# Performance work log

Hardware: AMD Instinct MI355X
Metric: run time of the kernel (lower is better)

## Reference

```python
import jax, jax.numpy as jnp
import numpy as np

HEADS = 8
DIM_HEAD = 64  # scale uses this, even though per-head dim is 128 (inner_dim = dim_head*heads*2)
SCALE = DIM_HEAD ** (-0.5)
QUERY_DIM = 1024
COND_DIM = 1024
INNER_DIM = DIM_HEAD * HEADS * 2  # 1024


def setup_inputs() -> dict:
    key = jax.random.key(0)
    ks = jax.random.split(key, 7)
    B, Nq, Nk = 4, 2048, 2048
    x = jax.random.normal(ks[0], (B, Nq, QUERY_DIM), dtype=jnp.float32)
    cond = jax.random.normal(ks[1], (B, Nk, COND_DIM), dtype=jnp.float32)
    s = 0.02
    Wq = jax.random.normal(ks[2], (QUERY_DIM, INNER_DIM), dtype=jnp.float32) * s
    Wk = jax.random.normal(ks[3], (COND_DIM, INNER_DIM), dtype=jnp.float32) * s
    Wv = jax.random.normal(ks[4], (COND_DIM, INNER_DIM), dtype=jnp.float32) * s
    Wo = jax.random.normal(ks[5], (INNER_DIM, QUERY_DIM), dtype=jnp.float32) * s
    bo = jax.random.normal(ks[6], (QUERY_DIM,), dtype=jnp.float32) * s
    return {"x": x, "cond": cond, "Wq": Wq, "Wk": Wk, "Wv": Wv, "Wo": Wo, "bo": bo}


def reference(x, cond, Wq, Wk, Wv, Wo, bo):
    B, Nq, _ = x.shape
    Nk = cond.shape[1]
    h = HEADS
    d = INNER_DIM // h  # 128 per-head dim
    q = (x @ Wq).reshape(B, Nq, h, d).transpose(0, 2, 1, 3)   # b h i d
    k = (cond @ Wk).reshape(B, Nk, h, d).transpose(0, 2, 1, 3)  # b h j d
    v = (cond @ Wv).reshape(B, Nk, h, d).transpose(0, 2, 1, 3)  # b h j d
    sim = jnp.einsum('bhid,bhjd->bhij', q, k) * SCALE
    attn = jax.nn.softmax(sim, axis=-1)
    out = jnp.einsum('bhij,bhjd->bhid', attn, v)
    out = out.transpose(0, 2, 1, 3).reshape(B, Nq, INNER_DIM)
    return out @ Wo + bo
```

## Files before the change

### kernel.cpp

```cpp
#include <hip/hip_runtime.h>
#include <cstdint>
#include <cstddef>


typedef __attribute__((ext_vector_type(8))) __bf16 bf16x8;
typedef __attribute__((ext_vector_type(4))) float  f32x4;

__device__ __forceinline__ unsigned short f2bf(float f) {
  union { float f; unsigned u; } v; v.f = f;
  unsigned r = v.u + 0x7FFFu + ((v.u >> 16) & 1u);
  return (unsigned short)(r >> 16);
}

__device__ __forceinline__ void async_copy16(const void* g, void* l) {
  __builtin_amdgcn_global_load_lds(
      (const __attribute__((address_space(1))) void*)g,
      (__attribute__((address_space(3))) void*)l, 16, 0, 0);
}

__device__ __forceinline__ void tile_ready_barrier() {
  __builtin_amdgcn_sched_barrier(0);
  asm volatile("s_waitcnt vmcnt(0)" ::: "memory");
  __builtin_amdgcn_s_barrier();
  __builtin_amdgcn_sched_barrier(0);
}

__global__ void convert2_f32_bf16(const float* __restrict__ a,
                                  unsigned short* __restrict__ ao,
                                  const float* __restrict__ b,
                                  unsigned short* __restrict__ bo, int n4) {
  const float* in = blockIdx.z ? b : a;
  unsigned short* out = blockIdx.z ? bo : ao;
  int idx = blockIdx.x * blockDim.x + threadIdx.x;
  int stride = gridDim.x * blockDim.x;
  for (int i = idx; i < n4; i += stride) {
    float4 v = ((const float4*)in)[i];
    ushort4 o;
    o.x = f2bf(v.x); o.y = f2bf(v.y); o.z = f2bf(v.z); o.w = f2bf(v.w);
    ((ushort4*)out)[i] = o;
  }
}

__global__ void tconv4(const float* __restrict__ W0, const float* __restrict__ W1,
                       const float* __restrict__ W2, const float* __restrict__ W3,
                       unsigned short* __restrict__ T0, unsigned short* __restrict__ T1,
                       unsigned short* __restrict__ T2, unsigned short* __restrict__ T3) {
  const int Kd = 1024, Nd = 1024;
  int z = blockIdx.z;
  const float* W = (z == 0) ? W0 : (z == 1) ? W1 : (z == 2) ? W2 : W3;
  unsigned short* Wt = (z == 0) ? T0 : (z == 1) ? T1 : (z == 2) ? T2 : T3;
  __shared__ float t[32][33];
  int tx = threadIdx.x, ty = threadIdx.y;
  int n0 = blockIdx.x * 32, k0 = blockIdx.y * 32;
#pragma unroll
  for (int i = 0; i < 4; ++i)
    t[ty + i * 8][tx] = W[(size_t)(k0 + ty + i * 8) * Nd + n0 + tx];
  __syncthreads();
#pragma unroll
  for (int i = 0; i < 4; ++i)
    Wt[(size_t)(n0 + ty + i * 8) * Kd + k0 + tx] = f2bf(t[tx][ty + i * 8]);
}

template <int MODE>
__global__ __launch_bounds__(256, 3) void gemm_bt(
    const unsigned short* __restrict__ A, const unsigned short* __restrict__ Bt,
    void* __restrict__ Cp, const float* __restrict__ bias, int M, int N, int Kd,
    float oscale) {
  __shared__ __align__(16) unsigned short As[2][128 * 32];
  __shared__ __align__(16) unsigned short Bs[2][128 * 32];
  int tid = threadIdx.x, lane = tid & 63, wid = tid >> 6;
  int wm = wid >> 1, wn = wid & 1;
  int nwg = gridDim.x * gridDim.y;
  int wg = blockIdx.y * gridDim.x + blockIdx.x;
  int cpx = nwg >> 3;
  int sw = (wg & 7) * cpx + (wg >> 3);
  int bx = sw % gridDim.x, by = sw / gridDim.x;
  int m0 = by * 128, n0 = bx * 128;
  int l15 = lane & 15, g = lane >> 4;
  const unsigned short* Ag = A + (size_t)m0 * Kd;
  const unsigned short* Bg = Bt + (size_t)n0 * Kd;
  f32x4 acc[4][4] = {};

  auto stage = [&](int buf, int k0) {
#pragma unroll
    for (int it = 0; it < 2; ++it) {
      int c = it * 256 + tid;
      int row = c >> 2, kg = c & 3;
      async_copy16(Ag + (size_t)row * Kd + k0 + kg * 8, &As[buf][c * 8]);
      async_copy16(Bg + (size_t)row * Kd + k0 + kg * 8, &Bs[buf][c * 8]);
    }
  };

  const int NT = Kd >> 5;
  stage(0, 0);

  for (int t = 0; t < NT; ++t) {
    tile_ready_barrier();
    if (t + 1 < NT) stage((t + 1) & 1, (t + 1) * 32);
    int cur = t & 1;
    bf16x8 af[4], bfr[4];
#pragma unroll
    for (int i = 0; i < 4; ++i) {
      af[i]  = *(const bf16x8*)(&As[cur][(wm * 64 + i * 16 + l15) * 32 + g * 8]);
      bfr[i] = *(const bf16x8*)(&Bs[cur][(wn * 64 + i * 16 + l15) * 32 + g * 8]);
    }
    __builtin_amdgcn_s_setprio(1);
#pragma unroll
    for (int i = 0; i < 4; ++i)
#pragma unroll
      for (int j = 0; j < 4; ++j)
        acc[i][j] = __builtin_amdgcn_mfma_f32_16x16x32_bf16(af[i], bfr[j], acc[i][j], 0, 0, 0);
    __builtin_amdgcn_s_setprio(0);
  }

#pragma unroll
  for (int i = 0; i < 4; ++i) {
#pragma unroll
    for (int j = 0; j < 4; ++j) {
#pragma unroll
      for (int r = 0; r < 4; ++r) {
        int row = m0 + wm * 64 + i * 16 + g * 4 + r;
        int col = n0 + wn * 64 + j * 16 + l15;
        float v = acc[i][j][r];
        if (MODE == 0) {
          ((unsigned short*)Cp)[(size_t)row * N + col] = f2bf(v * oscale);
        } else if (MODE == 1) {
          ((float*)Cp)[(size_t)row * N + col] = v + bias[col];
        } else {
          size_t off = ((size_t)((col >> 11) * 8 + (row >> 7)) << 18) +
                       (size_t)(row & 127) * 2048 + (size_t)(col & 2047);
          ((unsigned short*)Cp)[off] = f2bf(v);
        }
      }
    }
  }
}

#define KVB 64
#define NKV 2048

__global__ __launch_bounds__(512, 4) void attn_kernel(
    const unsigned short* __restrict__ Q, const unsigned short* __restrict__ K,
    const unsigned short* __restrict__ Vt, unsigned short* __restrict__ O) {
  __shared__ __align__(16) unsigned short Ks[2][KVB * 128];
  __shared__ __align__(16) unsigned short Vs[2][128 * KVB];
  __shared__ __align__(16) unsigned short Ps[8 * 16 * 64];

  int tid = threadIdx.x, lane = tid & 63, w = tid >> 6;
  int l15 = lane & 15, g = lane >> 4;
  int wgl = blockIdx.y * gridDim.x + blockIdx.x;
  int sw = (wgl & 7) * 64 + (wgl >> 3);
  int bh = sw >> 4, b = bh >> 3, h = bh & 7;
  int q0 = (sw & 15) * 128;

  const unsigned short* Qg = Q + ((size_t)(b * 2048 + q0 + w * 16)) * 1024 + h * 128;
  const unsigned short* Kg = K + ((size_t)(b * 2048)) * 1024 + h * 128;
  const unsigned short* Vg = Vt + (size_t)bh * (128 * 2048);

  bf16x8 qf[4];
#pragma unroll
  for (int kf = 0; kf < 4; ++kf)
    qf[kf] = *(const bf16x8*)(Qg + (size_t)l15 * 1024 + kf * 32 + g * 8);

  f32x4 of[8] = {};
  float mrun[4], lrun[4];
#pragma unroll
  for (int r = 0; r < 4; ++r) { mrun[r] = -1e30f; lrun[r] = 0.f; }

  auto stage = [&](int buf, int j0) {
#pragma unroll
    for (int it = 0; it < 2; ++it) {
      int c = it * 512 + tid;
      int row = c >> 4, kc = c & 15;
      async_copy16(Kg + (size_t)(j0 + row) * 1024 + ((kc ^ (row & 7)) * 8),
                   &Ks[buf][c * 8]);
    }
#pragma unroll
    for (int it = 0; it < 2; ++it) {
      int c = it * 512 + tid;
      int row = c >> 3, jc = c & 7;
      async_copy16(Vg + (size_t)row * 2048 + j0 + ((jc ^ (row & 7)) * 8),
                   &Vs[buf][c * 8]);
    }
  };

  const int NT = NKV / KVB;
  stage(0, 0);

  for (int t = 0; t < NT; ++t) {
    tile_ready_barrier();
    if (t + 1 < NT) stage((t + 1) & 1, (t + 1) * KVB);
    int cur = t & 1;

    f32x4 s[4] = {};
    __builtin_amdgcn_s_setprio(1);
#pragma unroll
    for (int jf = 0; jf < 4; ++jf) {
      int j = jf * 16 + l15;
#pragma unroll
      for (int kf = 0; kf < 4; ++kf) {
        bf16x8 kfr = *(const bf16x8*)(&Ks[cur][j * 128 + (((kf * 4 + g) ^ (j & 7)) * 8)]);
        s[jf] = __builtin_amdgcn_mfma_f32_16x16x32_bf16(qf[kf], kfr, s[jf], 0, 0, 0);
      }
    }
    __builtin_amdgcn_s_setprio(0);

#pragma unroll
    for (int r = 0; r < 4; ++r) {
      float mxl = fmaxf(fmaxf(s[0][r], s[1][r]), fmaxf(s[2][r], s[3][r]));
      if (!__all(mxl <= mrun[r] + 11.5f)) {
        float mx = mxl;
#pragma unroll
        for (int msk = 1; msk < 16; msk <<= 1) mx = fmaxf(mx, __shfl_xor(mx, msk, 64));
        float mnew = fmaxf(mrun[r], mx);
        float resc = __builtin_amdgcn_exp2f(mrun[r] - mnew);
        lrun[r] *= resc;
#pragma unroll
        for (int df = 0; df < 8; ++df) of[df][r] *= resc;
        mrun[r] = mnew;
      }
      float ps = 0.f;
      float pj[4];
#pragma unroll
      for (int jf = 0; jf < 4; ++jf) {
        pj[jf] = __builtin_amdgcn_exp2f(s[jf][r] - mrun[r]);
        ps += pj[jf];
      }
      lrun[r] += ps;
      int prow = g * 4 + r;
#pragma unroll
      for (int jf = 0; jf < 4; ++jf) {
        int idx = (w * 16 + prow) * 64 +
                  (((jf * 2 + (l15 >> 3)) ^ (prow & 7)) << 3) + (l15 & 7);
        Ps[idx] = f2bf(pj[jf]);
      }
    }

    bf16x8 pa[2];
#pragma unroll
    for (int kf2 = 0; kf2 < 2; ++kf2)
      pa[kf2] = *(const bf16x8*)(&Ps[(w * 16 + l15) * 64 + (((kf2 * 4 + g) ^ (l15 & 7)) << 3)]);
    __builtin_amdgcn_s_setprio(1);
#pragma unroll
    for (int df = 0; df < 8; ++df) {
      int d = df * 16 + l15;
#pragma unroll
      for (int kf2 = 0; kf2 < 2; ++kf2) {
        bf16x8 vfr = *(const bf16x8*)(&Vs[cur][d * 64 + (((kf2 * 4 + g) ^ (d & 7)) * 8)]);
        of[df] = __builtin_amdgcn_mfma_f32_16x16x32_bf16(pa[kf2], vfr, of[df], 0, 0, 0);
      }
    }
    __builtin_amdgcn_s_setprio(0);
  }

  float inv[4];
#pragma unroll
  for (int r = 0; r < 4; ++r) {
    float ps = lrun[r];
#pragma unroll
    for (int msk = 1; msk < 16; msk <<= 1) ps += __shfl_xor(ps, msk, 64);
    inv[r] = 1.0f / ps;
  }
  unsigned short* Og = O + ((size_t)(b * 2048 + q0 + w * 16)) * 1024 + h * 128;
#pragma unroll
  for (int df = 0; df < 8; ++df)
#pragma unroll
    for (int r = 0; r < 4; ++r)
      Og[(size_t)(g * 4 + r) * 1024 + df * 16 + l15] = f2bf(of[df][r] * inv[r]);
}

extern "C" void kernel_launch(void* const* d_in, const int* in_sizes, int n_in,
                              void* d_out, int out_size, void* d_ws, size_t ws_size,
                              hipStream_t stream) {
  const float* x    = (const float*)d_in[0];
  const float* cond = (const float*)d_in[1];
  const float* Wq   = (const float*)d_in[2];
  const float* Wk   = (const float*)d_in[3];
  const float* Wv   = (const float*)d_in[4];
  const float* Wo   = (const float*)d_in[5];
  const float* bo   = (const float*)d_in[6];

  char* p = (char*)d_ws;
  unsigned short* xb  = (unsigned short*)(p + 0);
  unsigned short* cb  = (unsigned short*)(p + 16777216);
  unsigned short* Wqt = (unsigned short*)(p + 33554432);
  unsigned short* Wkt = (unsigned short*)(p + 35651584);
  unsigned short* Wvt = (unsigned short*)(p + 37748736);
  unsigned short* Wot = (unsigned short*)(p + 39845888);
  unsigned short* Qb  = (unsigned short*)(p + 41943040);
  unsigned short* Kb  = (unsigned short*)(p + 58720256);
  unsigned short* Vtb = (unsigned short*)(p + 75497472);
  unsigned short* Ab  = (unsigned short*)(p + 92274688);
  (void)in_sizes; (void)n_in; (void)out_size; (void)ws_size;

  convert2_f32_bf16<<<dim3(1024, 1, 2), 256, 0, stream>>>(x, xb, cond, cb, 8388608 / 4);
  tconv4<<<dim3(32, 32, 4), dim3(32, 8), 0, stream>>>(Wq, Wk, Wv, Wo, Wqt, Wkt, Wvt, Wot);

  const float QSCALE = 0.125f * 1.44269504f;

  gemm_bt<0><<<dim3(8, 64), 256, 0, stream>>>(xb, Wqt, Qb, nullptr, 8192, 1024, 1024, QSCALE);
  gemm_bt<0><<<dim3(8, 64), 256, 0, stream>>>(cb, Wkt, Kb, nullptr, 8192, 1024, 1024, 1.0f);
  gemm_bt<2><<<dim3(64, 8), 256, 0, stream>>>(Wvt, cb, Vtb, nullptr, 1024, 8192, 1024, 1.0f);

  attn_kernel<<<dim3(16, 32), 512, 0, stream>>>(Qb, Kb, Vtb, Ab);

  gemm_bt<1><<<dim3(8, 64), 256, 0, stream>>>(Ab, Wot, (float*)d_out, bo, 8192, 1024, 1024, 1.0f);
}
```

Baseline: 329.0 us.

## Merge Q and K projection GEMMs, XOR-swizzle LDS tiles, raise GEMM occupancy

Folds the Q and K projections into one launch by treating the contiguous Wqt and Wkt buffers as a single 2048-row B matrix. Each block picks its A source and output buffer from its column tile. The GEMM also gets an XOR swizzle on the k-chunk placement in LDS to cut bank conflicts on fragment reads, a fixed grouped block-to-tile mapping, and launch bounds raised from 3 to 4 blocks per CU. It removes one launch and improves LDS read efficiency, but relies on the workspace layout keeping Wqt and Wkt adjacent.

Result: faster. 313.8 us (-4.6%).

```diff
diff --git a/kernel.cpp b/kernel.cpp
--- a/kernel.cpp
+++ b/kernel.cpp
@@ -62,22 +62,26 @@
 }
 
 template <int MODE>
-__global__ __launch_bounds__(256, 3) void gemm_bt(
-    const unsigned short* __restrict__ A, const unsigned short* __restrict__ Bt,
-    void* __restrict__ Cp, const float* __restrict__ bias, int M, int N, int Kd,
-    float oscale) {
+__global__ __launch_bounds__(256, 4) void gemm5(
+    const unsigned short* __restrict__ A0, const unsigned short* __restrict__ A1,
+    const unsigned short* __restrict__ Bt, void* __restrict__ C0,
+    void* __restrict__ C1, const float* __restrict__ bias, float qscale) {
+  const int Kd = 1024;
   __shared__ __align__(16) unsigned short As[2][128 * 32];
   __shared__ __align__(16) unsigned short Bs[2][128 * 32];
   int tid = threadIdx.x, lane = tid & 63, wid = tid >> 6;
   int wm = wid >> 1, wn = wid & 1;
-  int nwg = gridDim.x * gridDim.y;
+  int l15 = lane & 15, g = lane >> 4;
+
   int wg = blockIdx.y * gridDim.x + blockIdx.x;
-  int cpx = nwg >> 3;
-  int sw = (wg & 7) * cpx + (wg >> 3);
-  int bx = sw % gridDim.x, by = sw / gridDim.x;
+  int x = wg & 7, i = wg >> 3;
+  int bx, by;
+  if (MODE == 2) { bx = x * 8 + (i >> 3); by = i & 7; }
+  else           { bx = i >> 3;           by = x * 8 + (i & 7); }
   int m0 = by * 128, n0 = bx * 128;
-  int l15 = lane & 15, g = lane >> 4;
-  const unsigned short* Ag = A + (size_t)m0 * Kd;
+
+  const unsigned short* Asrc = (MODE == 0 && n0 >= 1024) ? A1 : A0;
+  const unsigned short* Ag = Asrc + (size_t)m0 * Kd;
   const unsigned short* Bg = Bt + (size_t)n0 * Kd;
   f32x4 acc[4][4] = {};
 
@@ -86,50 +90,55 @@
     for (int it = 0; it < 2; ++it) {
       int c = it * 256 + tid;
       int row = c >> 2, kg = c & 3;
-      async_copy16(Ag + (size_t)row * Kd + k0 + kg * 8, &As[buf][c * 8]);
-      async_copy16(Bg + (size_t)row * Kd + k0 + kg * 8, &Bs[buf][c * 8]);
+      int ks = kg ^ ((row >> 1) & 3);
+      async_copy16(Ag + (size_t)row * Kd + k0 + ks * 8, &As[buf][c * 8]);
+      async_copy16(Bg + (size_t)row * Kd + k0 + ks * 8, &Bs[buf][c * 8]);
     }
   };
 
   const int NT = Kd >> 5;
   stage(0, 0);
 
+  int rsw = (g ^ ((l15 >> 1) & 3)) * 8;
   for (int t = 0; t < NT; ++t) {
     tile_ready_barrier();
     if (t + 1 < NT) stage((t + 1) & 1, (t + 1) * 32);
     int cur = t & 1;
     bf16x8 af[4], bfr[4];
 #pragma unroll
-    for (int i = 0; i < 4; ++i) {
-      af[i]  = *(const bf16x8*)(&As[cur][(wm * 64 + i * 16 + l15) * 32 + g * 8]);
-      bfr[i] = *(const bf16x8*)(&Bs[cur][(wn * 64 + i * 16 + l15) * 32 + g * 8]);
+    for (int ii = 0; ii < 4; ++ii) {
+      af[ii]  = *(const bf16x8*)(&As[cur][(wm * 64 + ii * 16 + l15) * 32 + rsw]);
+      bfr[ii] = *(const bf16x8*)(&Bs[cur][(wn * 64 + ii * 16 + l15) * 32 + rsw]);
     }
     __builtin_amdgcn_s_setprio(1);
 #pragma unroll
-    for (int i = 0; i < 4; ++i)
-#pragma unroll
-      for (int j = 0; j < 4; ++j)
-        acc[i][j] = __builtin_amdgcn_mfma_f32_16x16x32_bf16(af[i], bfr[j], acc[i][j], 0, 0, 0);
+    for (int ii = 0; ii < 4; ++ii)
+#pragma unroll
+      for (int jj = 0; jj < 4; ++jj)
+        acc[ii][jj] = __builtin_amdgcn_mfma_f32_16x16x32_bf16(af[ii], bfr[jj], acc[ii][jj], 0, 0, 0);
     __builtin_amdgcn_s_setprio(0);
   }
 
 #pragma unroll
-  for (int i = 0; i < 4; ++i) {
-#pragma unroll
-    for (int j = 0; j < 4; ++j) {
+  for (int ii = 0; ii < 4; ++ii) {
+#pragma unroll
+    for (int jj = 0; jj < 4; ++jj) {
 #pragma unroll
       for (int r = 0; r < 4; ++r) {
-        int row = m0 + wm * 64 + i * 16 + g * 4 + r;
-        int col = n0 + wn * 64 + j * 16 + l15;
-        float v = acc[i][j][r];
+        int row = m0 + wm * 64 + ii * 16 + g * 4 + r;
+        int col = n0 + wn * 64 + jj * 16 + l15;
+        float v = acc[ii][jj][r];
         if (MODE == 0) {
-          ((unsigned short*)Cp)[(size_t)row * N + col] = f2bf(v * oscale);
+          if (n0 < 1024)
+            ((unsigned short*)C0)[(size_t)row * 1024 + col] = f2bf(v * qscale);
+          else
+            ((unsigned short*)C1)[(size_t)row * 1024 + (col & 1023)] = f2bf(v);
         } else if (MODE == 1) {
-          ((float*)Cp)[(size_t)row * N + col] = v + bias[col];
+          ((float*)C0)[(size_t)row * 1024 + col] = v + bias[col];
         } else {
           size_t off = ((size_t)((col >> 11) * 8 + (row >> 7)) << 18) +
                        (size_t)(row & 127) * 2048 + (size_t)(col & 2047);
-          ((unsigned short*)Cp)[off] = f2bf(v);
+          ((unsigned short*)C0)[off] = f2bf(v);
         }
       }
     }
@@ -298,11 +307,10 @@
 
   const float QSCALE = 0.125f * 1.44269504f;
 
-  gemm_bt<0><<<dim3(8, 64), 256, 0, stream>>>(xb, Wqt, Qb, nullptr, 8192, 1024, 1024, QSCALE);
-  gemm_bt<0><<<dim3(8, 64), 256, 0, stream>>>(cb, Wkt, Kb, nullptr, 8192, 1024, 1024, 1.0f);
-  gemm_bt<2><<<dim3(64, 8), 256, 0, stream>>>(Wvt, cb, Vtb, nullptr, 1024, 8192, 1024, 1.0f);
+  gemm5<0><<<dim3(16, 64), 256, 0, stream>>>(xb, cb, Wqt, Qb, Kb, nullptr, QSCALE);
+  gemm5<2><<<dim3(64, 8), 256, 0, stream>>>(Wvt, nullptr, cb, Vtb, nullptr, nullptr, 1.0f);
 
   attn_kernel<<<dim3(16, 32), 512, 0, stream>>>(Qb, Kb, Vtb, Ab);
 
-  gemm_bt<1><<<dim3(8, 64), 256, 0, stream>>>(Ab, Wot, (float*)d_out, bo, 8192, 1024, 1024, 1.0f);
-}
+  gemm5<1><<<dim3(8, 64), 256, 0, stream>>>(Ab, nullptr, Wot, (float*)d_out, nullptr, bo, 1.0f);
+}
```
